# Kernel optimization log

Hardware: AMD Instinct MI355X
Metric: run time of the kernel (lower is better)

## Reference

```python
import jax, jax.numpy as jnp
import numpy as np

H, HEAD_DIM = 12, 64
D = H * HEAD_DIM  # 768
SCALE = HEAD_DIM ** -0.5


def setup_inputs() -> dict:
    key = jax.random.key(0)
    ks = jax.random.split(key, 8)
    B, N, M, C = 2, 2048, 2048, 768
    s = 0.02
    return {
        "x": jax.random.normal(ks[0], (B, N, C), jnp.float32),
        "src": jax.random.normal(ks[1], (B, M, C), jnp.float32),
        "qk_w": jax.random.normal(ks[2], (2 * D, C), jnp.float32) * s,
        "qk_src_w": jax.random.normal(ks[3], (2 * D, C), jnp.float32) * s,
        "v_w": jax.random.normal(ks[4], (D, C), jnp.float32) * s,
        "v_src_w": jax.random.normal(ks[5], (D, C), jnp.float32) * s,
        "proj_w": jax.random.normal(ks[6], (C, D), jnp.float32) * s,
        "proj_b": jnp.zeros((C,), jnp.float32),
        "proj_src_w": jax.random.normal(ks[7], (C, D), jnp.float32) * s,
        "proj_src_b": jnp.zeros((C,), jnp.float32),
    }


def reference(x, src, qk_w, qk_src_w, v_w, v_src_w, proj_w, proj_b, proj_src_w, proj_src_b):
    B, N, _ = x.shape
    M = src.shape[1]

    def split_heads(t):  # [B, L, H*dh] -> [B, H, L, dh]
        return t.reshape(B, -1, H, t.shape[-1] // H).transpose(0, 2, 1, 3)

    qk = split_heads(x @ qk_w.T)          # [B,H,N,2*HEAD_DIM]
    qk_s = split_heads(src @ qk_src_w.T)  # [B,H,M,2*HEAD_DIM]
    v = split_heads(x @ v_w.T)            # [B,H,N,HEAD_DIM]
    v_s = split_heads(src @ v_src_w.T)    # [B,H,M,HEAD_DIM]

    # shared similarity: computed once, softmaxed along both directions
    sim = jnp.einsum('bhnd,bhmd->bhnm', qk * SCALE, qk_s)  # [B,H,N,M]
    attn = jax.nn.softmax(sim, axis=-1)      # x -> src (rows)
    attn_src = jax.nn.softmax(sim, axis=-2)  # src -> x (columns)

    y = jnp.einsum('bhnm,bhmd->bhnd', attn, v_s)       # [B,H,N,dh]
    y_src = jnp.einsum('bhnm,bhnd->bhmd', attn_src, v)  # [B,H,M,dh]

    merge = lambda t: t.transpose(0, 2, 1, 3).reshape(B, -1, D)
    y = merge(y) @ proj_w.T + proj_b
    y_src = merge(y_src) @ proj_src_w.T + proj_src_b
    return jnp.concatenate([y, y_src], axis=-1)  # [B, N, out+out_src]
```

## Files before the change

### kernel.cpp

```cpp
#include <hip/hip_runtime.h>
#include <hip/hip_bf16.h>
#include <cstdint>
#include <cstddef>


typedef __attribute__((ext_vector_type(4))) float f32x4;
typedef __attribute__((ext_vector_type(8))) short bf16x8;
typedef __attribute__((ext_vector_type(4))) short s16x4;
typedef __attribute__((ext_vector_type(4))) unsigned int u32x4;

__device__ __forceinline__ short f2bf(float f) {
  union { float f; unsigned u; } v; v.f = f;
  unsigned r = v.u + 0x7FFF + ((v.u >> 16) & 1);
  return (short)(r >> 16);
}

__device__ __forceinline__ unsigned cvt_pk_bf16(float lo, float hi) {
  unsigned r;
  asm("v_cvt_pk_bf16_f32 %0, %1, %2" : "=v"(r) : "v"(lo), "v"(hi));
  return r;
}

__device__ __forceinline__ void async16(const void* g, void* l) {
  __builtin_amdgcn_global_load_lds(
      (__attribute__((address_space(1))) unsigned int*)(g),
      (__attribute__((address_space(3))) unsigned int*)(l),
      16, 0, 0);
}

__global__ __launch_bounds__(256)
void cvt_all(const float* __restrict__ x, const float* __restrict__ src,
             const float* __restrict__ qkw, const float* __restrict__ qksw,
             const float* __restrict__ vw, const float* __restrict__ vsw,
             const float* __restrict__ pw, const float* __restrict__ psw,
             short* __restrict__ out) {
  int i = blockIdx.x * 256 + threadIdx.x;
  const float* in; int local; float scale = 1.f;
  if (i < 1572864) {
    if (i < 786432) { in = x; local = i; } else { in = src; local = i - 786432; }
  } else if (i < 2162688) {
    if (i < 1867776) { in = qkw; local = i - 1572864; scale = 0.125f * 1.44269504f; }
    else             { in = qksw; local = i - 1867776; }
  } else if (i < 2457600) {
    if (i < 2310144) { in = vw; local = i - 2162688; } else { in = vsw; local = i - 2310144; }
  } else {
    if (i < 2605056) { in = pw; local = i - 2457600; } else { in = psw; local = i - 2605056; }
  }
  float4 v = ((const float4*)in)[local];
  s16x4 o = { f2bf(v.x * scale), f2bf(v.y * scale),
              f2bf(v.z * scale), f2bf(v.w * scale) };
  ((s16x4*)out)[i] = o;
}

enum { EPI_HEAD128 = 0, EPI_HEADT64 = 1, EPI_PROJ = 2 };

template<int EPI, int TR>
__device__ __forceinline__
void gemm_core(short* As, short* Ws,
               const short* __restrict__ A, const short* __restrict__ W,
               short* __restrict__ outb, const float* __restrict__ bias,
               float* __restrict__ outf, int outColOff, int bx, int by) {
  constexpr int NI = TR / 32;
  const int tid  = threadIdx.x;
  const int lane = tid & 63, wid = tid >> 6;
  const int wr = wid >> 1, wc = wid & 1;
  const int rowBase = by * TR, colBase = bx << 7;
  const int c = lane & 15, g = lane >> 4;

  constexpr int AROWS = (TR == 128) ? 32 : 16;
  const short* gA = A + (size_t)(rowBase + wid * AROWS + (lane >> 2)) * 768 + (lane & 3) * 8;
  const short* gW = W + (size_t)(colBase + wid * 32 + (lane >> 2)) * 768 + (lane & 3) * 8;
  short* lA = As + wid * AROWS * 32;
  short* lW = Ws + wid * 32 * 32;

  const short* rA = As + (wr * (TR / 2) + c) * 32 + g * 8;
  const short* rW = Ws + (wc * 64 + c) * 32 + g * 8;

  f32x4 acc[NI][4] = {};

  for (int kt = 0; kt < 24; ++kt) {
    async16(gA, lA);
    if (TR == 128) async16(gA + 16 * 768, lA + 16 * 32);
    async16(gW,            lW);
    async16(gW + 16 * 768, lW + 16 * 32);
    gA += 32; gW += 32;
    __syncthreads();
    bf16x8 af[NI], wf[4];
#pragma unroll
    for (int i = 0; i < NI; ++i) af[i] = *(const bf16x8*)(rA + i * 512);
#pragma unroll
    for (int j = 0; j < 4; ++j) wf[j] = *(const bf16x8*)(rW + j * 512);
#pragma unroll
    for (int i = 0; i < NI; ++i)
#pragma unroll
      for (int j = 0; j < 4; ++j)
        acc[i][j] = __builtin_amdgcn_mfma_f32_16x16x32_bf16(af[i], wf[j], acc[i][j], 0, 0, 0);
    __syncthreads();
  }

  if (EPI == EPI_HEAD128) {
#pragma unroll
    for (int i = 0; i < NI; ++i) {
      int row = rowBase + wr * (TR / 2) + i * 16 + g * 4;
      int b = row >> 11, n = row & 2047;
#pragma unroll
      for (int j = 0; j < 4; ++j) {
        int f = colBase + wc * 64 + j * 16 + c;
        int h = f >> 7, d = f & 127;
        short* p = outb + ((size_t)(b * 12 + h) * 2048 + n) * 128 + d;
#pragma unroll
        for (int r = 0; r < 4; ++r) p[(size_t)r * 128] = f2bf(acc[i][j][r]);
      }
    }
  } else if (EPI == EPI_HEADT64) {
#pragma unroll
    for (int i = 0; i < NI; ++i) {
      int row = rowBase + wr * (TR / 2) + i * 16 + g * 4;
      int b = row >> 11, n = row & 2047;
#pragma unroll
      for (int j = 0; j < 4; ++j) {
        int f = colBase + wc * 64 + j * 16 + c;
        int h = f >> 6, d = f & 63;
        s16x4 o4 = { f2bf(acc[i][j][0]), f2bf(acc[i][j][1]),
                     f2bf(acc[i][j][2]), f2bf(acc[i][j][3]) };
        *(s16x4*)(outb + ((size_t)(b * 12 + h) * 64 + d) * 2048 + n) = o4;
      }
    }
  } else {
#pragma unroll
    for (int j = 0; j < 4; ++j) {
      int colj = colBase + wc * 64 + j * 16 + c;
      float bv = bias[colj];
#pragma unroll
      for (int i = 0; i < NI; ++i) {
        int row = rowBase + wr * (TR / 2) + i * 16 + g * 4;
#pragma unroll
        for (int r = 0; r < 4; ++r)
          outf[(size_t)(row + r) * 1536 + outColOff + colj] = acc[i][j][r] + bv;
      }
    }
  }
}

__global__ __launch_bounds__(256)
void gemm_in_fused(const short* __restrict__ xb, const short* __restrict__ qkwb,
                   short* __restrict__ qk, const short* __restrict__ sb,
                   const short* __restrict__ qkswb, short* __restrict__ qks,
                   const short* __restrict__ vwb, short* __restrict__ vT,
                   const short* __restrict__ vswb, short* __restrict__ vsT) {
  __shared__ short As[128 * 32];
  __shared__ short Ws[128 * 32];
  const int bid = blockIdx.x;
  if (bid < 768) {
    const int bx = bid % 12, y = bid / 12;
    const int sel = y >> 5, by = y & 31;
    gemm_core<EPI_HEAD128, 128>(As, Ws, sel ? sb : xb, sel ? qkswb : qkwb,
                                sel ? qks : qk, nullptr, nullptr, 0, bx, by);
  } else {
    const int t = bid - 768;
    const int bx = t % 6, y = t / 6;
    const int sel = y >> 6, by = y & 63;
    gemm_core<EPI_HEADT64, 64>(As, Ws, sel ? sb : xb, sel ? vswb : vwb,
                               sel ? vsT : vT, nullptr, nullptr, 0, bx, by);
  }
}

__global__ __launch_bounds__(256)
void gemm_proj(const short* __restrict__ A0, const short* __restrict__ W0,
               const float* __restrict__ bias0,
               const short* __restrict__ A1, const short* __restrict__ W1,
               const float* __restrict__ bias1, float* __restrict__ outf) {
  __shared__ short As[64 * 32];
  __shared__ short Ws[128 * 32];
  const int sel = blockIdx.y >> 6;
  const int by  = blockIdx.y & 63;
  gemm_core<EPI_PROJ, 64>(As, Ws, sel ? A1 : A0, sel ? W1 : W0, nullptr,
                          sel ? bias1 : bias0, outf, sel ? 768 : 0,
                          blockIdx.x, by);
}

__global__ __launch_bounds__(256)
void attn_fwd(const short* __restrict__ Q0, const short* __restrict__ K0,
              const short* __restrict__ Vt0, short* __restrict__ Y0,
              const short* __restrict__ Q1, const short* __restrict__ K1,
              const short* __restrict__ Vt1, short* __restrict__ Y1) {
  __shared__ short Ks[64 * 136];
  __shared__ short Vs[64 * 72];

  const int dir = blockIdx.y >= 24;
  const int bh  = dir ? blockIdx.y - 24 : blockIdx.y;
  const short* Qg  = dir ? Q1 : Q0;
  const short* Kg  = dir ? K1 : K0;
  const short* Vtg = dir ? Vt1 : Vt0;
  short* Y         = dir ? Y1 : Y0;

  const int tid = threadIdx.x, lane = tid & 63, wid = tid >> 6;
  const int c = lane & 15, g = lane >> 4;
  const int b = bh / 12, h = bh % 12;
  const int q0 = blockIdx.x * 128 + wid * 32;

  bf16x8 qf[2][4];
#pragma unroll
  for (int qb = 0; qb < 2; ++qb) {
    const short* qp = Qg + ((size_t)bh * 2048 + q0 + qb * 16 + c) * 128 + g * 8;
#pragma unroll
    for (int kk = 0; kk < 4; ++kk) qf[qb][kk] = *(const bf16x8*)(qp + kk * 32);
  }

  f32x4 o[2][4];
#pragma unroll
  for (int qb = 0; qb < 2; ++qb)
#pragma unroll
    for (int db = 0; db < 4; ++db) o[qb][db] = f32x4{0.f, 0.f, 0.f, 0.f};
  float lsumP[2] = {0.f, 0.f};

  const short* kbase = Kg + (size_t)bh * 2048 * 128;
  const short* vbase = Vtg + (size_t)bh * 64 * 2048;

  const int srow = tid >> 2, scc = (tid & 3) * 32, skc = (tid & 3) * 16;

  bf16x8 kreg[4], vreg[2];
  auto gload = [&](int kt) {
    const short* srcK = kbase + ((size_t)(kt * 64 + srow)) * 128 + scc;
#pragma unroll
    for (int u = 0; u < 4; ++u) kreg[u] = *(const bf16x8*)(srcK + u * 8);
    const short* srcV = vbase + (size_t)srow * 2048 + kt * 64 + skc;
    vreg[0] = *(const bf16x8*)(srcV);
    vreg[1] = *(const bf16x8*)(srcV + 8);
  };
  auto lwrite = [&]() {
    short* dstK = Ks + srow * 136 + scc;
#pragma unroll
    for (int u = 0; u < 4; ++u) *(bf16x8*)(dstK + u * 8) = kreg[u];
    short* dstV = Vs + srow * 72 + skc;
    *(bf16x8*)(dstV)     = vreg[0];
    *(bf16x8*)(dstV + 8) = vreg[1];
  };

  gload(0);
  for (int kt = 0; kt < 32; ++kt) {
    lwrite();
    __syncthreads();

    f32x4 st[2][4];
#pragma unroll
    for (int qb = 0; qb < 2; ++qb)
#pragma unroll
      for (int j = 0; j < 4; ++j) st[qb][j] = f32x4{0.f, 0.f, 0.f, 0.f};
#pragma unroll
    for (int j = 0; j < 4; ++j)
#pragma unroll
      for (int kk = 0; kk < 4; ++kk) {
        bf16x8 kf = *(const bf16x8*)(Ks + (j * 16 + c) * 136 + kk * 32 + g * 8);
        st[0][j] = __builtin_amdgcn_mfma_f32_16x16x32_bf16(kf, qf[0][kk], st[0][j], 0, 0, 0);
        st[1][j] = __builtin_amdgcn_mfma_f32_16x16x32_bf16(kf, qf[1][kk], st[1][j], 0, 0, 0);
      }

    bf16x8 pa[2][2];
#pragma unroll
    for (int qb = 0; qb < 2; ++qb) {
      float p[4][4];
#pragma unroll
      for (int j = 0; j < 4; ++j)
#pragma unroll
        for (int r = 0; r < 4; ++r) p[j][r] = exp2f(st[qb][j][r]);
      float s0 = (p[0][0] + p[0][1]) + (p[0][2] + p[0][3]);
      float s1 = (p[1][0] + p[1][1]) + (p[1][2] + p[1][3]);
      float s2 = (p[2][0] + p[2][1]) + (p[2][2] + p[2][3]);
      float s3 = (p[3][0] + p[3][1]) + (p[3][2] + p[3][3]);
      lsumP[qb] += (s0 + s1) + (s2 + s3);
#pragma unroll
      for (int kb = 0; kb < 2; ++kb) {
        union { u32x4 u; bf16x8 v; } pk;
        pk.u[0] = cvt_pk_bf16(p[2 * kb][0],     p[2 * kb][1]);
        pk.u[1] = cvt_pk_bf16(p[2 * kb][2],     p[2 * kb][3]);
        pk.u[2] = cvt_pk_bf16(p[2 * kb + 1][0], p[2 * kb + 1][1]);
        pk.u[3] = cvt_pk_bf16(p[2 * kb + 1][2], p[2 * kb + 1][3]);
        pa[qb][kb] = pk.v;
      }
    }

    if (kt + 1 < 32) gload(kt + 1);

#pragma unroll
    for (int kb = 0; kb < 2; ++kb)
#pragma unroll
      for (int db = 0; db < 4; ++db) {
        union { s16x4 h[2]; bf16x8 v; } vf;
        const short* vrow = Vs + (size_t)(db * 16 + c) * 72 + kb * 32 + g * 4;
        vf.h[0] = *(const s16x4*)(vrow);
        vf.h[1] = *(const s16x4*)(vrow + 16);
        o[0][db] = __builtin_amdgcn_mfma_f32_16x16x32_bf16(pa[0][kb], vf.v, o[0][db], 0, 0, 0);
        o[1][db] = __builtin_amdgcn_mfma_f32_16x16x32_bf16(pa[1][kb], vf.v, o[1][db], 0, 0, 0);
      }
    __syncthreads();
  }

  float L[2];
#pragma unroll
  for (int qb = 0; qb < 2; ++qb) {
    float v = lsumP[qb];
    v += __shfl_xor(v, 16, 64);
    v += __shfl_xor(v, 32, 64);
    L[qb] = v;
  }
#pragma unroll
  for (int qb = 0; qb < 2; ++qb) {
    float inv[4];
#pragma unroll
    for (int r = 0; r < 4; ++r)
      inv[r] = 1.0f / __shfl(L[qb], g * 4 + r, 64);
    short* yp = Y + ((size_t)(b * 2048) + q0 + qb * 16 + g * 4) * 768 + h * 64 + c;
#pragma unroll
    for (int db = 0; db < 4; ++db)
#pragma unroll
      for (int r = 0; r < 4; ++r)
        yp[(size_t)r * 768 + db * 16] = f2bf(o[qb][db][r] * inv[r]);
  }
}

extern "C" void kernel_launch(void* const* d_in, const int* in_sizes, int n_in,
                              void* d_out, int out_size, void* d_ws, size_t ws_size,
                              hipStream_t stream) {
  (void)in_sizes; (void)n_in; (void)out_size; (void)ws_size;

  const float* x     = (const float*)d_in[0];
  const float* srcp  = (const float*)d_in[1];
  const float* qk_w  = (const float*)d_in[2];
  const float* qks_w = (const float*)d_in[3];
  const float* v_w   = (const float*)d_in[4];
  const float* vs_w  = (const float*)d_in[5];
  const float* p_w   = (const float*)d_in[6];
  const float* p_b   = (const float*)d_in[7];
  const float* ps_w  = (const float*)d_in[8];
  const float* ps_b  = (const float*)d_in[9];
  float* out = (float*)d_out;

  char* ws = (char*)d_ws;
  size_t off = 0;
  auto alloc = [&](size_t elems) -> short* {
    short* p = (short*)(ws + off);
    off += (elems * 2 + 255) & ~(size_t)255;
    return p;
  };
  short* xb    = alloc(4096UL * 768);
  short* sb    = alloc(4096UL * 768);
  short* qkwb  = alloc(1536UL * 768);
  short* qkswb = alloc(1536UL * 768);
  short* vwb   = alloc(768UL * 768);
  short* vswb  = alloc(768UL * 768);
  short* pwb   = alloc(768UL * 768);
  short* pswb  = alloc(768UL * 768);
  short* qk    = alloc(24UL * 2048 * 128);
  short* qks   = alloc(24UL * 2048 * 128);
  short* vT    = alloc(24UL * 64 * 2048);
  short* vsT   = alloc(24UL * 64 * 2048);
  short* y     = alloc(4096UL * 768);
  short* ysv   = alloc(4096UL * 768);

  cvt_all<<<dim3(10752), dim3(256), 0, stream>>>(x, srcp, qk_w, qks_w, v_w, vs_w,
                                                 p_w, ps_w, xb);

  gemm_in_fused<<<dim3(1536), 256, 0, stream>>>(xb, qkwb, qk, sb, qkswb, qks,
                                                vwb, vT, vswb, vsT);

  attn_fwd<<<dim3(16, 48), 256, 0, stream>>>(qk, qks, vsT, y,
                                             qks, qk, vT, ysv);

  gemm_proj<<<dim3(6, 128), 256, 0, stream>>>(y, pwb, p_b, ysv, pswb, ps_b, out);
}
```

Before: 197.1 us.

## Switch attention inner loops to 32x32x16 MFMA with permlane32 swap for P

Replaces the 16x16x32 MFMA tiling in the attention kernel with 32x32x16 MFMA tiles, so each wave holds 32 query rows as one block and processes the 64-key tile in two 32-key halves. The probability tile is repacked from the S accumulator layout into the A-operand layout using v_permlane32_swap rather than being rebuilt from 16x16 fragments. The aim is fewer MFMA issues and fewer LDS fragment reads per FLOP. The cost is a changed register layout, extra lane swaps, and a reworked output indexing and normalization path.

Result: faster. 188.4 us (median of 2 runs) (-4.4%).

```diff
diff --git a/kernel.cpp b/kernel.cpp
--- a/kernel.cpp
+++ b/kernel.cpp
@@ -5,6 +5,7 @@
 
 
 typedef __attribute__((ext_vector_type(4))) float f32x4;
+typedef __attribute__((ext_vector_type(16))) float f32x16;
 typedef __attribute__((ext_vector_type(8))) short bf16x8;
 typedef __attribute__((ext_vector_type(4))) short s16x4;
 typedef __attribute__((ext_vector_type(4))) unsigned int u32x4;
@@ -19,6 +20,10 @@
   unsigned r;
   asm("v_cvt_pk_bf16_f32 %0, %1, %2" : "=v"(r) : "v"(lo), "v"(hi));
   return r;
+}
+
+__device__ __forceinline__ void permlane32_swap(unsigned &a, unsigned &b) {
+  asm volatile("v_permlane32_swap_b32 %0, %1" : "+v"(a), "+v"(b));
 }
 
 __device__ __forceinline__ void async16(const void* g, void* l) {
@@ -195,24 +200,19 @@
   short* Y         = dir ? Y1 : Y0;
 
   const int tid = threadIdx.x, lane = tid & 63, wid = tid >> 6;
-  const int c = lane & 15, g = lane >> 4;
-  const int b = bh / 12, h = bh % 12;
+  const int m31 = lane & 31, lh = lane >> 5;
+  const int b = bh / 12, head = bh % 12;
   const int q0 = blockIdx.x * 128 + wid * 32;
 
-  bf16x8 qf[2][4];
-#pragma unroll
-  for (int qb = 0; qb < 2; ++qb) {
-    const short* qp = Qg + ((size_t)bh * 2048 + q0 + qb * 16 + c) * 128 + g * 8;
-#pragma unroll
-    for (int kk = 0; kk < 4; ++kk) qf[qb][kk] = *(const bf16x8*)(qp + kk * 32);
-  }
-
-  f32x4 o[2][4];
-#pragma unroll
-  for (int qb = 0; qb < 2; ++qb)
-#pragma unroll
-    for (int db = 0; db < 4; ++db) o[qb][db] = f32x4{0.f, 0.f, 0.f, 0.f};
-  float lsumP[2] = {0.f, 0.f};
+  bf16x8 qf[8];
+  {
+    const short* qp = Qg + ((size_t)bh * 2048 + q0 + m31) * 128 + lh * 8;
+#pragma unroll
+    for (int kd = 0; kd < 8; ++kd) qf[kd] = *(const bf16x8*)(qp + kd * 16);
+  }
+
+  f32x16 o[2] = {};
+  float lsumP = 0.f;
 
   const short* kbase = Kg + (size_t)bh * 2048 * 128;
   const short* vbase = Vtg + (size_t)bh * 64 * 2048;
@@ -242,80 +242,70 @@
     lwrite();
     __syncthreads();
 
-    f32x4 st[2][4];
-#pragma unroll
-    for (int qb = 0; qb < 2; ++qb)
-#pragma unroll
-      for (int j = 0; j < 4; ++j) st[qb][j] = f32x4{0.f, 0.f, 0.f, 0.f};
-#pragma unroll
-    for (int j = 0; j < 4; ++j)
-#pragma unroll
-      for (int kk = 0; kk < 4; ++kk) {
-        bf16x8 kf = *(const bf16x8*)(Ks + (j * 16 + c) * 136 + kk * 32 + g * 8);
-        st[0][j] = __builtin_amdgcn_mfma_f32_16x16x32_bf16(kf, qf[0][kk], st[0][j], 0, 0, 0);
-        st[1][j] = __builtin_amdgcn_mfma_f32_16x16x32_bf16(kf, qf[1][kk], st[1][j], 0, 0, 0);
-      }
-
-    bf16x8 pa[2][2];
-#pragma unroll
-    for (int qb = 0; qb < 2; ++qb) {
-      float p[4][4];
-#pragma unroll
-      for (int j = 0; j < 4; ++j)
-#pragma unroll
-        for (int r = 0; r < 4; ++r) p[j][r] = exp2f(st[qb][j][r]);
-      float s0 = (p[0][0] + p[0][1]) + (p[0][2] + p[0][3]);
-      float s1 = (p[1][0] + p[1][1]) + (p[1][2] + p[1][3]);
-      float s2 = (p[2][0] + p[2][1]) + (p[2][2] + p[2][3]);
-      float s3 = (p[3][0] + p[3][1]) + (p[3][2] + p[3][3]);
-      lsumP[qb] += (s0 + s1) + (s2 + s3);
-#pragma unroll
-      for (int kb = 0; kb < 2; ++kb) {
+#pragma unroll
+    for (int kt2 = 0; kt2 < 2; ++kt2) {
+      f32x16 st = {};
+#pragma unroll
+      for (int kd = 0; kd < 8; ++kd) {
+        bf16x8 kf = *(const bf16x8*)(Ks + (kt2 * 32 + m31) * 136 + kd * 16 + lh * 8);
+        st = __builtin_amdgcn_mfma_f32_32x32x16_bf16(kf, qf[kd], st, 0, 0, 0);
+      }
+
+      float p[16];
+#pragma unroll
+      for (int r = 0; r < 16; ++r) p[r] = exp2f(st[r]);
+      lsumP += (((p[0] + p[1]) + (p[2] + p[3])) + ((p[4] + p[5]) + (p[6] + p[7])))
+             + (((p[8] + p[9]) + (p[10] + p[11])) + ((p[12] + p[13]) + (p[14] + p[15])));
+
+      unsigned wlo[4], whi[4];
+#pragma unroll
+      for (int j = 0; j < 4; ++j) {
+        wlo[j] = cvt_pk_bf16(p[4 * j],     p[4 * j + 1]);
+        whi[j] = cvt_pk_bf16(p[4 * j + 2], p[4 * j + 3]);
+      }
+      bf16x8 pa[2];
+#pragma unroll
+      for (int t = 0; t < 2; ++t) {
+        unsigned a0 = wlo[2 * t], b0 = wlo[2 * t + 1];
+        unsigned a1 = whi[2 * t], b1 = whi[2 * t + 1];
+        permlane32_swap(a0, b0);
+        permlane32_swap(a1, b1);
         union { u32x4 u; bf16x8 v; } pk;
-        pk.u[0] = cvt_pk_bf16(p[2 * kb][0],     p[2 * kb][1]);
-        pk.u[1] = cvt_pk_bf16(p[2 * kb][2],     p[2 * kb][3]);
-        pk.u[2] = cvt_pk_bf16(p[2 * kb + 1][0], p[2 * kb + 1][1]);
-        pk.u[3] = cvt_pk_bf16(p[2 * kb + 1][2], p[2 * kb + 1][3]);
-        pa[qb][kb] = pk.v;
-      }
-    }
-
-    if (kt + 1 < 32) gload(kt + 1);
-
-#pragma unroll
-    for (int kb = 0; kb < 2; ++kb)
-#pragma unroll
-      for (int db = 0; db < 4; ++db) {
-        union { s16x4 h[2]; bf16x8 v; } vf;
-        const short* vrow = Vs + (size_t)(db * 16 + c) * 72 + kb * 32 + g * 4;
-        vf.h[0] = *(const s16x4*)(vrow);
-        vf.h[1] = *(const s16x4*)(vrow + 16);
-        o[0][db] = __builtin_amdgcn_mfma_f32_16x16x32_bf16(pa[0][kb], vf.v, o[0][db], 0, 0, 0);
-        o[1][db] = __builtin_amdgcn_mfma_f32_16x16x32_bf16(pa[1][kb], vf.v, o[1][db], 0, 0, 0);
-      }
+        pk.u[0] = a0; pk.u[1] = a1; pk.u[2] = b0; pk.u[3] = b1;
+        pa[t] = pk.v;
+      }
+
+      if (kt2 == 1 && kt + 1 < 32) gload(kt + 1);
+
+#pragma unroll
+      for (int t = 0; t < 2; ++t)
+#pragma unroll
+        for (int dt = 0; dt < 2; ++dt) {
+          bf16x8 vf = *(const bf16x8*)(Vs + (size_t)(dt * 32 + m31) * 72
+                                       + (kt2 * 2 + t) * 16 + lh * 8);
+          o[dt] = __builtin_amdgcn_mfma_f32_32x32x16_bf16(pa[t], vf, o[dt], 0, 0, 0);
+        }
+    }
     __syncthreads();
   }
 
-  float L[2];
-#pragma unroll
-  for (int qb = 0; qb < 2; ++qb) {
-    float v = lsumP[qb];
-    v += __shfl_xor(v, 16, 64);
-    v += __shfl_xor(v, 32, 64);
-    L[qb] = v;
-  }
-#pragma unroll
-  for (int qb = 0; qb < 2; ++qb) {
-    float inv[4];
-#pragma unroll
-    for (int r = 0; r < 4; ++r)
-      inv[r] = 1.0f / __shfl(L[qb], g * 4 + r, 64);
-    short* yp = Y + ((size_t)(b * 2048) + q0 + qb * 16 + g * 4) * 768 + h * 64 + c;
-#pragma unroll
-    for (int db = 0; db < 4; ++db)
-#pragma unroll
-      for (int r = 0; r < 4; ++r)
-        yp[(size_t)r * 768 + db * 16] = f2bf(o[qb][db][r] * inv[r]);
+  float L = lsumP;
+  L += __shfl_xor(L, 32, 64);
+
+  float inv[16];
+#pragma unroll
+  for (int r = 0; r < 16; ++r) {
+    int qr = (r & 3) + 8 * (r >> 2) + 4 * lh;
+    inv[r] = 1.0f / __shfl(L, qr, 64);
+  }
+#pragma unroll
+  for (int dt = 0; dt < 2; ++dt) {
+    short* yp = Y + ((size_t)(b * 2048) + q0) * 768 + head * 64 + dt * 32 + m31;
+#pragma unroll
+    for (int r = 0; r < 16; ++r) {
+      int qr = (r & 3) + 8 * (r >> 2) + 4 * lh;
+      yp[(size_t)qr * 768] = f2bf(o[dt][r] * inv[r]);
+    }
   }
 }
 
```
